# Performance work log

Measured on AMD Instinct MI355X. Metric: run time of the kernel, lower is better.

Reference implementation:

```python
import jax, jax.numpy as jnp
import numpy as np

H = 16
D_MODEL = 1024
D_K = D_MODEL // H


def setup_inputs() -> dict:
    key = jax.random.key(0)
    ks = jax.random.split(key, 12)
    B, S = 4, 2048
    scale = 1.0 / np.sqrt(D_MODEL)
    inp = {
        "query": jax.random.normal(ks[0], (B, S, D_MODEL), dtype=jnp.float32),
        "key": jax.random.normal(ks[1], (B, S, D_MODEL), dtype=jnp.float32),
        "value": jax.random.normal(ks[2], (B, S, D_MODEL), dtype=jnp.float32),
        "Wq": jax.random.normal(ks[3], (D_MODEL, D_MODEL), dtype=jnp.float32) * scale,
        "bq": jnp.zeros((D_MODEL,), dtype=jnp.float32),
        "Wk": jax.random.normal(ks[4], (D_MODEL, D_MODEL), dtype=jnp.float32) * scale,
        "bk": jnp.zeros((D_MODEL,), dtype=jnp.float32),
        "Wv": jax.random.normal(ks[5], (D_MODEL, D_MODEL), dtype=jnp.float32) * scale,
        "bv": jnp.zeros((D_MODEL,), dtype=jnp.float32),
        "Wo": jax.random.normal(ks[6], (D_MODEL, D_MODEL), dtype=jnp.float32) * scale,
        "bo": jnp.zeros((D_MODEL,), dtype=jnp.float32),
    }
    return inp


def reference(query, key, value, Wq, bq, Wk, bk, Wv, bv, Wo, bo):
    B, S, _ = query.shape
    # Linear projections (torch Linear: x @ W^T + b), then split heads -> [B,H,S,d_k]
    def proj(x, W, b):
        y = x @ W.T + b
        return y.reshape(B, S, H, D_K).transpose(0, 2, 1, 3)

    q = proj(query, Wq, bq)
    k = proj(key, Wk, bk)
    v = proj(value, Wv, bv)

    # Explicit QK^T / sqrt(d_k), softmax, AV (no mask; dropout = identity in eval)
    scores = jnp.einsum("bhqd,bhkd->bhqk", q, k) / jnp.sqrt(jnp.float32(D_K))
    attn = jax.nn.softmax(scores, axis=-1)
    x = jnp.einsum("bhqk,bhkd->bhqd", attn, v)

    # Merge heads and final output projection
    x = x.transpose(0, 2, 1, 3).reshape(B, S, H * D_K)
    return x @ Wo.T + bo
```

## Files before the change

### kernel.cpp

```cpp
#include <hip/hip_runtime.h>
#include <hip/hip_bf16.h>
#include <stdint.h>

#define BATCH 4
#define SEQ   2048
#define DM    1024
#define NH    16
#define DK    64
#define MROWS (BATCH * SEQ)

#define C1 0.1803368801111204f

typedef __attribute__((ext_vector_type(8))) short short8;
typedef __attribute__((ext_vector_type(4))) float f32x4;
typedef __attribute__((ext_vector_type(4))) float floatv4;
typedef __attribute__((ext_vector_type(4))) unsigned short us4;
typedef __attribute__((ext_vector_type(4))) unsigned int uint4v;

static __device__ __forceinline__ unsigned short f2bf(float f) {
    union { float f; uint32_t u; } c; c.f = f;
    uint32_t u = c.u;
    return (unsigned short)((u + 0x7fffu + ((u >> 16) & 1u)) >> 16);
}

static __device__ __forceinline__ unsigned int cvt_pk_bf16(float a, float b) {
    __hip_bfloat162 h = __float22bfloat162_rn(float2{a, b});
    unsigned int u; __builtin_memcpy(&u, &h, 4); return u;
}

static __device__ __forceinline__ float ex2(float x) { return __builtin_amdgcn_exp2f(x); }

#define AS1C(p) ((const __attribute__((address_space(1))) unsigned int*)(uintptr_t)(const void*)(p))
#define AS3(p)  ((__attribute__((address_space(3))) unsigned int*)(uintptr_t)(void*)(p))

__global__ __launch_bounds__(256) void cvt3_k(const float* __restrict__ a, const float* __restrict__ b,
                                              const float* __restrict__ c,
                                              unsigned short* __restrict__ oa, unsigned short* __restrict__ ob,
                                              unsigned short* __restrict__ oc) {
    const int z = blockIdx.y;
    const float* s = (z == 0) ? a : (z == 1) ? b : c;
    unsigned short* o = (z == 0) ? oa : (z == 1) ? ob : oc;
    int i = blockIdx.x * 256 + threadIdx.x;
    floatv4 v = ((const floatv4*)s)[i];
    us4 w; w.x = f2bf(v.x); w.y = f2bf(v.y); w.z = f2bf(v.z); w.w = f2bf(v.w);
    ((us4*)o)[i] = w;
}

__global__ __launch_bounds__(256) void cvt4_k(const float* __restrict__ a, const float* __restrict__ b,
                                              const float* __restrict__ c, const float* __restrict__ d,
                                              unsigned short* __restrict__ oa, unsigned short* __restrict__ ob,
                                              unsigned short* __restrict__ oc, unsigned short* __restrict__ od) {
    const int z = blockIdx.y;
    const float* s = (z == 0) ? a : (z == 1) ? b : (z == 2) ? c : d;
    unsigned short* o = (z == 0) ? oa : (z == 1) ? ob : (z == 2) ? oc : od;
    int i = blockIdx.x * 256 + threadIdx.x;
    floatv4 v = ((const floatv4*)s)[i];
    us4 w; w.x = f2bf(v.x); w.y = f2bf(v.y); w.z = f2bf(v.z); w.w = f2bf(v.w);
    ((us4*)o)[i] = w;
}

static __device__ __forceinline__ void gemm_body(const unsigned short* __restrict__ A,
                                                 const unsigned short* __restrict__ Bw,
                                                 const float* __restrict__ bias,
                                                 void* __restrict__ out, int m0, int n0,
                                                 float scale, int mode) {
    constexpr int K = DM;
    constexpr int NK = K / 32;

    const int tid = threadIdx.x;
    const int wave = tid >> 6, lane = tid & 63, quad = lane >> 4, l16 = lane & 15;
    const int wm = wave >> 1, wn = wave & 1;

    __shared__ alignas(16) unsigned short As[2][256 * 32];
    __shared__ alignas(16) unsigned short Bs[2][128 * 32];

    f32x4 acc[4][4];
    #pragma unroll
    for (int i = 0; i < 4; i++)
        #pragma unroll
        for (int j = 0; j < 4; j++) acc[i][j] = (f32x4){0.f, 0.f, 0.f, 0.f};

    const int scol8 = (((lane & 3) ^ ((lane >> 3) & 3))) * 8;
    const unsigned short* Ag0 = A  + (size_t)(m0 + wave * 32 + (lane >> 2)) * K + scol8;
    const unsigned short* Ag1 = Ag0 + (size_t)16 * K;
    const unsigned short* Bg0 = Bw + (size_t)(n0 + wave * 16 + (lane >> 2)) * K + scol8;

    const int rsw = (quad ^ ((l16 >> 1) & 3)) * 8;

    short8 af[4], bfr[4];

#define GX_STG(b, kt)                                                                     \
    {   __builtin_amdgcn_global_load_lds(AS1C(Ag0 + (size_t)(kt) * 32),                   \
                                         AS3(&As[b][(wave * 32) * 32]), 16, 0, 0);        \
        __builtin_amdgcn_global_load_lds(AS1C(Ag1 + (size_t)(kt) * 32),                   \
                                         AS3(&As[b][(wave * 32 + 16) * 32]), 16, 0, 0);   \
        __builtin_amdgcn_global_load_lds(AS1C(Bg0 + (size_t)(kt) * 32),                   \
                                         AS3(&Bs[b][(wave * 16) * 32]), 16, 0, 0); }

#define GX_LD(b)                                                                          \
    {   _Pragma("unroll")                                                                 \
        for (int i_ = 0; i_ < 4; i_++) af[i_]  = *(const short8*)&As[b][(wm * 64 + i_ * 16 + l16) * 32 + rsw]; \
        _Pragma("unroll")                                                                 \
        for (int j_ = 0; j_ < 4; j_++) bfr[j_] = *(const short8*)&Bs[b][(wn * 64 + j_ * 16 + l16) * 32 + rsw]; }

#define GX_MMA                                                                            \
    {   __builtin_amdgcn_s_setprio(1);                                                    \
        _Pragma("unroll")                                                                 \
        for (int i_ = 0; i_ < 4; i_++)                                                    \
            _Pragma("unroll")                                                             \
            for (int j_ = 0; j_ < 4; j_++)                                                \
                acc[i_][j_] = __builtin_amdgcn_mfma_f32_16x16x32_bf16(af[i_], bfr[j_], acc[i_][j_], 0, 0, 0); \
        __builtin_amdgcn_s_setprio(0); }

#define GX_VM0  { asm volatile("s_waitcnt vmcnt(0)" ::: "memory"); }
#define GX_BAR  __builtin_amdgcn_s_barrier()
#define GX_SB0  __builtin_amdgcn_sched_barrier(0)
#define GX_LG0  { asm volatile("s_waitcnt lgkmcnt(0)" ::: "memory"); __builtin_amdgcn_sched_barrier(0); }

    GX_STG(0, 0);
    #pragma unroll 1
    for (int k = 0; k < NK; k += 2) {
        GX_VM0; GX_BAR; GX_SB0;
        GX_STG(1, k + 1);
        GX_LD(0); GX_LG0; GX_MMA;
        GX_VM0; GX_BAR; GX_SB0;
        if (k + 2 < NK) GX_STG(0, k + 2);
        GX_LD(1); GX_LG0; GX_MMA;
    }

#undef GX_STG
#undef GX_LD
#undef GX_MMA
#undef GX_VM0
#undef GX_BAR
#undef GX_SB0
#undef GX_LG0

    #pragma unroll
    for (int nf = 0; nf < 4; nf++) {
        const int n = n0 + wn * 64 + nf * 16 + l16;
        const float bv = bias[n];
        if (mode == 2) {
            const int bb = m0 >> 11;
            const int hh = n >> 6, dd = n & (DK - 1);
            unsigned short* obase = (unsigned short*)out
                                  + (((size_t)bb * NH + hh) * DK + dd) * SEQ
                                  + (m0 & (SEQ - 1)) + wm * 64 + quad * 8;
            #pragma unroll
            for (int mf = 0; mf < 4; mf++) {
                us4 w;
                #pragma unroll
                for (int r = 0; r < 4; r++) w[r] = f2bf(acc[mf][nf][r] + bv);
                *(us4*)(obase + (mf >> 1) * 32 + (mf & 1) * 4) = w;
            }
        } else {
            const int hh = n >> 6, dd = n & (DK - 1);
            #pragma unroll
            for (int mf = 0; mf < 4; mf++) {
                #pragma unroll
                for (int r = 0; r < 4; r++) {
                    const int mrow = m0 + wm * 64 + mf * 16 + quad * 4 + r;
                    float val = (acc[mf][nf][r] + bv) * scale;
                    if (mode == 0) {
                        int bb = mrow >> 11, ss = mrow & (SEQ - 1);
                        ((unsigned short*)out)[((((size_t)bb * NH + hh) * SEQ + ss) << 6) + dd] = f2bf(val);
                    } else {
                        ((float*)out)[(size_t)mrow * DM + n] = val;
                    }
                }
            }
        }
    }
}

__global__ __launch_bounds__(512, 4) void gemm_qkv_k(const unsigned short* qa, const unsigned short* ka,
                                                     const unsigned short* va, const unsigned short* wq,
                                                     const unsigned short* wk, const unsigned short* wv,
                                                     const float* bq, const float* bk, const float* bv,
                                                     unsigned short* qh, unsigned short* kh,
                                                     unsigned short* vtc) {
    const int z = blockIdx.z;
    const unsigned short* A = (z == 0) ? qa : (z == 1) ? ka : va;
    const unsigned short* W = (z == 0) ? wq : (z == 1) ? wk : wv;
    const float* bi = (z == 0) ? bq : (z == 1) ? bk : bv;
    void* o = (z == 0) ? (void*)qh : (z == 1) ? (void*)kh : (void*)vtc;
    const float sc = (z == 0) ? C1 : 1.0f;
    const int mode = (z == 2) ? 2 : 0;
    gemm_body(A, W, bi, o, blockIdx.x * 256, blockIdx.y * 128, sc, mode);
}

__global__ __launch_bounds__(512, 4) void gemm_o_k(const unsigned short* xb, const unsigned short* wo,
                                                   const float* bo, float* out) {
    gemm_body(xb, wo, bo, out, blockIdx.x * 256, blockIdx.y * 128, 1.0f, 1);
}

__global__ __launch_bounds__(256, 2) void flash_attn_k(const unsigned short* __restrict__ Qh,
                                                       const unsigned short* __restrict__ Kh,
                                                       const unsigned short* __restrict__ Vtc,
                                                       unsigned short* __restrict__ Xb) {
    const int tid = threadIdx.x;
    const int wave = tid >> 6, lane = tid & 63, quad = lane >> 4, l16 = lane & 15;
    const int h = blockIdx.y, b = blockIdx.z;
    const unsigned short* Qp = Qh  + (size_t)(b * NH + h) * SEQ * DK;
    const unsigned short* Kp = Kh  + (size_t)(b * NH + h) * SEQ * DK;
    const unsigned short* Vp = Vtc + (size_t)(b * NH + h) * DK * SEQ;
    const int q0 = blockIdx.x * 256 + wave * 64;

    __shared__ alignas(16) unsigned short kt[128][72];
    __shared__ alignas(16) unsigned short vt[64][136];

    short8 aq[4][2];
    #pragma unroll
    for (int m = 0; m < 4; m++)
        #pragma unroll
        for (int kk = 0; kk < 2; kk++)
            aq[m][kk] = *(const short8*)(Qp + (size_t)(q0 + m * 16 + l16) * DK + kk * 32 + quad * 8);

    short8 ones;
    #pragma unroll
    for (int j = 0; j < 8; j++) ones[j] = (short)0x3F80;

    f32x4 O[4][4];
    f32x4 lacc[4];
    #pragma unroll
    for (int m = 0; m < 4; m++) {
        #pragma unroll
        for (int db = 0; db < 4; db++) O[m][db] = (f32x4){0.f, 0.f, 0.f, 0.f};
        lacc[m] = (f32x4){0.f, 0.f, 0.f, 0.f};
    }

    const unsigned short* kgp = Kp + (size_t)(tid >> 3) * DK + (tid & 7) * 8;
    const unsigned short* vgp = Vp + (size_t)(tid >> 4) * SEQ + (tid & 15) * 8;
    unsigned short* kws = &kt[tid >> 3][(tid & 7) * 8];
    unsigned short* vws = &vt[tid >> 4][(tid & 15) * 8];

    short8 krg[4], vrg[4];
    #pragma unroll
    for (int it = 0; it < 4; it++) {
        krg[it] = *(const short8*)(kgp + (size_t)it * 32 * DK);
        vrg[it] = *(const short8*)(vgp + (size_t)it * 16 * SEQ);
    }
    kgp += (size_t)128 * DK;
    vgp += 128;

    for (int t0 = 0; t0 < SEQ; t0 += 128) {
        __syncthreads();
        #pragma unroll
        for (int it = 0; it < 4; it++) {
            *(short8*)(kws + it * 32 * 72) = krg[it];
            *(short8*)(vws + it * 16 * 136) = vrg[it];
        }
        #pragma unroll
        for (int it = 0; it < 4; it++) {
            krg[it] = *(const short8*)(kgp + (size_t)it * 32 * DK);
            vrg[it] = *(const short8*)(vgp + (size_t)it * 16 * SEQ);
        }
        kgp += (size_t)128 * DK;
        vgp += 128;
        asm volatile("s_waitcnt lgkmcnt(0)" ::: "memory");
        __builtin_amdgcn_s_barrier();
        __builtin_amdgcn_sched_barrier(0);

        #pragma unroll
        for (int t = 0; t < 4; t++) {
            f32x4 s[4][2];
            #pragma unroll
            for (int m = 0; m < 4; m++)
                #pragma unroll
                for (int sb = 0; sb < 2; sb++) s[m][sb] = (f32x4){0.f, 0.f, 0.f, 0.f};

            #pragma unroll
            for (int kk = 0; kk < 2; kk++) {
                short8 bk0 = *(const short8*)&kt[(t * 2    ) * 16 + l16][kk * 32 + quad * 8];
                short8 bk1 = *(const short8*)&kt[(t * 2 + 1) * 16 + l16][kk * 32 + quad * 8];
                #pragma unroll
                for (int m = 0; m < 4; m++) {
                    s[m][0] = __builtin_amdgcn_mfma_f32_16x16x32_bf16(bk0, aq[m][kk], s[m][0], 0, 0, 0);
                    s[m][1] = __builtin_amdgcn_mfma_f32_16x16x32_bf16(bk1, aq[m][kk], s[m][1], 0, 0, 0);
                }
            }

            short8 pa[4];
            #pragma unroll
            for (int m = 0; m < 4; m++) {
                uint4v pk;
                pk.x = cvt_pk_bf16(ex2(s[m][0][0]), ex2(s[m][0][1]));
                pk.y = cvt_pk_bf16(ex2(s[m][0][2]), ex2(s[m][0][3]));
                pk.z = cvt_pk_bf16(ex2(s[m][1][0]), ex2(s[m][1][1]));
                pk.w = cvt_pk_bf16(ex2(s[m][1][2]), ex2(s[m][1][3]));
                __builtin_memcpy(&pa[m], &pk, 16);
            }

            #pragma unroll
            for (int db = 0; db < 4; db++) {
                short8 vf = *(const short8*)&vt[db * 16 + l16][t * 32 + quad * 8];
                #pragma unroll
                for (int m = 0; m < 4; m++)
                    O[m][db] = __builtin_amdgcn_mfma_f32_16x16x32_bf16(pa[m], vf, O[m][db], 0, 0, 0);
            }
            #pragma unroll
            for (int m = 0; m < 4; m++)
                lacc[m] = __builtin_amdgcn_mfma_f32_16x16x32_bf16(pa[m], ones, lacc[m], 0, 0, 0);
        }
    }

    #pragma unroll
    for (int m = 0; m < 4; m++) {
        #pragma unroll
        for (int r = 0; r < 4; r++) {
            const float inv = 1.f / lacc[m][r];
            const int srow = q0 + m * 16 + quad * 4 + r;
            unsigned short* op = Xb + ((size_t)b * SEQ + srow) * DM + h * DK;
            #pragma unroll
            for (int db = 0; db < 4; db++)
                op[db * 16 + l16] = f2bf(O[m][db][r] * inv);
        }
    }
}

extern "C" void kernel_launch(void* const* d_in, const int* in_sizes, int n_in,
                              void* d_out, int out_size, void* d_ws, size_t ws_size,
                              hipStream_t stream) {
    const float* q_in = (const float*)d_in[0];
    const float* k_in = (const float*)d_in[1];
    const float* v_in = (const float*)d_in[2];
    const float* Wq   = (const float*)d_in[3];
    const float* bq   = (const float*)d_in[4];
    const float* Wk   = (const float*)d_in[5];
    const float* bk   = (const float*)d_in[6];
    const float* Wv   = (const float*)d_in[7];
    const float* bv   = (const float*)d_in[8];
    const float* Wo   = (const float*)d_in[9];
    const float* bo   = (const float*)d_in[10];

    const size_t MB = 1024ull * 1024ull;
    char* ws = (char*)d_ws;
    unsigned short* qa  = (unsigned short*)(ws +   0 * MB);
    unsigned short* ka  = (unsigned short*)(ws +  16 * MB);
    unsigned short* va  = (unsigned short*)(ws +  32 * MB);
    unsigned short* wqb = (unsigned short*)(ws +  48 * MB);
    unsigned short* wkb = (unsigned short*)(ws +  50 * MB);
    unsigned short* wvb = (unsigned short*)(ws +  52 * MB);
    unsigned short* wob = (unsigned short*)(ws +  54 * MB);
    unsigned short* qh  = (unsigned short*)(ws +  56 * MB);
    unsigned short* kh  = (unsigned short*)(ws +  72 * MB);
    unsigned short* vtc = (unsigned short*)(ws +  88 * MB);
    unsigned short* xb  = (unsigned short*)(ws + 104 * MB);

    cvt3_k<<<dim3(8192, 3), 256, 0, stream>>>(q_in, k_in, v_in, qa, ka, va);
    cvt4_k<<<dim3(1024, 4), 256, 0, stream>>>(Wq, Wk, Wv, Wo, wqb, wkb, wvb, wob);

    gemm_qkv_k<<<dim3(MROWS / 256, DM / 128, 3), 512, 0, stream>>>(qa, ka, va, wqb, wkb, wvb,
                                                                   bq, bk, bv, qh, kh, vtc);

    flash_attn_k<<<dim3(SEQ / 256, NH, BATCH), 256, 0, stream>>>(qh, kh, vtc, xb);

    gemm_o_k<<<dim3(MROWS / 256, DM / 128), 512, 0, stream>>>(xb, wob, bo, (float*)d_out);
}
```

Baseline: 327.0 us.

## Double-buffer K/V tiles in flash attention and merge conversion kernels

The flash attention kernel now keeps two LDS buffers for K and V. The next tile is written into the alternate buffer while the current one is consumed, so each tile needs one barrier instead of two. The two fp32-to-bf16 conversion kernels are also merged into a single launch, which saves one launch overhead. The cost is double the attention LDS use (about 36KB per block), which could limit occupancy, plus an extra prefetch past the end of the sequence on the last tiles.

```diff
diff --git a/kernel.cpp b/kernel.cpp
--- a/kernel.cpp
+++ b/kernel.cpp
@@ -33,29 +33,32 @@
 #define AS1C(p) ((const __attribute__((address_space(1))) unsigned int*)(uintptr_t)(const void*)(p))
 #define AS3(p)  ((__attribute__((address_space(3))) unsigned int*)(uintptr_t)(void*)(p))
 
-__global__ __launch_bounds__(256) void cvt3_k(const float* __restrict__ a, const float* __restrict__ b,
-                                              const float* __restrict__ c,
-                                              unsigned short* __restrict__ oa, unsigned short* __restrict__ ob,
-                                              unsigned short* __restrict__ oc) {
-    const int z = blockIdx.y;
-    const float* s = (z == 0) ? a : (z == 1) ? b : c;
-    unsigned short* o = (z == 0) ? oa : (z == 1) ? ob : oc;
-    int i = blockIdx.x * 256 + threadIdx.x;
-    floatv4 v = ((const floatv4*)s)[i];
-    us4 w; w.x = f2bf(v.x); w.y = f2bf(v.y); w.z = f2bf(v.z); w.w = f2bf(v.w);
-    ((us4*)o)[i] = w;
-}
-
-__global__ __launch_bounds__(256) void cvt4_k(const float* __restrict__ a, const float* __restrict__ b,
-                                              const float* __restrict__ c, const float* __restrict__ d,
-                                              unsigned short* __restrict__ oa, unsigned short* __restrict__ ob,
-                                              unsigned short* __restrict__ oc, unsigned short* __restrict__ od) {
-    const int z = blockIdx.y;
-    const float* s = (z == 0) ? a : (z == 1) ? b : (z == 2) ? c : d;
-    unsigned short* o = (z == 0) ? oa : (z == 1) ? ob : (z == 2) ? oc : od;
-    int i = blockIdx.x * 256 + threadIdx.x;
-    floatv4 v = ((const floatv4*)s)[i];
-    us4 w; w.x = f2bf(v.x); w.y = f2bf(v.y); w.z = f2bf(v.z); w.w = f2bf(v.w);
+__global__ __launch_bounds__(256) void cvt_k(const float* __restrict__ q, const float* __restrict__ k,
+                                             const float* __restrict__ v, const float* __restrict__ wq,
+                                             const float* __restrict__ wk, const float* __restrict__ wv,
+                                             const float* __restrict__ wo,
+                                             unsigned short* __restrict__ oq, unsigned short* __restrict__ ok,
+                                             unsigned short* __restrict__ ov, unsigned short* __restrict__ owq,
+                                             unsigned short* __restrict__ owk, unsigned short* __restrict__ owv,
+                                             unsigned short* __restrict__ owo) {
+    const int bid = blockIdx.x;
+    const float* s;
+    unsigned short* o;
+    int i;
+    if (bid < 24576) {
+        const int z = bid >> 13;
+        i = (bid & 8191) * 256 + threadIdx.x;
+        s = (z == 0) ? q : (z == 1) ? k : v;
+        o = (z == 0) ? oq : (z == 1) ? ok : ov;
+    } else {
+        const int r = bid - 24576;
+        const int z = r >> 10;
+        i = (r & 1023) * 256 + threadIdx.x;
+        s = (z == 0) ? wq : (z == 1) ? wk : (z == 2) ? wv : wo;
+        o = (z == 0) ? owq : (z == 1) ? owk : (z == 2) ? owv : owo;
+    }
+    floatv4 vv = ((const floatv4*)s)[i];
+    us4 w; w.x = f2bf(vv.x); w.y = f2bf(vv.y); w.z = f2bf(vv.z); w.w = f2bf(vv.w);
     ((us4*)o)[i] = w;
 }
 
@@ -206,8 +209,8 @@
     const unsigned short* Vp = Vtc + (size_t)(b * NH + h) * DK * SEQ;
     const int q0 = blockIdx.x * 256 + wave * 64;
 
-    __shared__ alignas(16) unsigned short kt[128][72];
-    __shared__ alignas(16) unsigned short vt[64][136];
+    __shared__ alignas(16) unsigned short kt[2][128][72];
+    __shared__ alignas(16) unsigned short vt[2][64][136];
 
     short8 aq[4][2];
     #pragma unroll
@@ -231,8 +234,8 @@
 
     const unsigned short* kgp = Kp + (size_t)(tid >> 3) * DK + (tid & 7) * 8;
     const unsigned short* vgp = Vp + (size_t)(tid >> 4) * SEQ + (tid & 15) * 8;
-    unsigned short* kws = &kt[tid >> 3][(tid & 7) * 8];
-    unsigned short* vws = &vt[tid >> 4][(tid & 15) * 8];
+    unsigned short* kws0 = &kt[0][tid >> 3][(tid & 7) * 8];
+    unsigned short* vws0 = &vt[0][tid >> 4][(tid & 15) * 8];
 
     short8 krg[4], vrg[4];
     #pragma unroll
@@ -242,67 +245,85 @@
     }
     kgp += (size_t)128 * DK;
     vgp += 128;
-
-    for (int t0 = 0; t0 < SEQ; t0 += 128) {
-        __syncthreads();
-        #pragma unroll
-        for (int it = 0; it < 4; it++) {
-            *(short8*)(kws + it * 32 * 72) = krg[it];
-            *(short8*)(vws + it * 16 * 136) = vrg[it];
-        }
-        #pragma unroll
-        for (int it = 0; it < 4; it++) {
-            krg[it] = *(const short8*)(kgp + (size_t)it * 32 * DK);
-            vrg[it] = *(const short8*)(vgp + (size_t)it * 16 * SEQ);
-        }
-        kgp += (size_t)128 * DK;
-        vgp += 128;
-        asm volatile("s_waitcnt lgkmcnt(0)" ::: "memory");
-        __builtin_amdgcn_s_barrier();
-        __builtin_amdgcn_sched_barrier(0);
-
-        #pragma unroll
-        for (int t = 0; t < 4; t++) {
-            f32x4 s[4][2];
-            #pragma unroll
-            for (int m = 0; m < 4; m++)
-                #pragma unroll
-                for (int sb = 0; sb < 2; sb++) s[m][sb] = (f32x4){0.f, 0.f, 0.f, 0.f};
-
-            #pragma unroll
-            for (int kk = 0; kk < 2; kk++) {
-                short8 bk0 = *(const short8*)&kt[(t * 2    ) * 16 + l16][kk * 32 + quad * 8];
-                short8 bk1 = *(const short8*)&kt[(t * 2 + 1) * 16 + l16][kk * 32 + quad * 8];
-                #pragma unroll
-                for (int m = 0; m < 4; m++) {
-                    s[m][0] = __builtin_amdgcn_mfma_f32_16x16x32_bf16(bk0, aq[m][kk], s[m][0], 0, 0, 0);
-                    s[m][1] = __builtin_amdgcn_mfma_f32_16x16x32_bf16(bk1, aq[m][kk], s[m][1], 0, 0, 0);
-                }
-            }
-
-            short8 pa[4];
-            #pragma unroll
-            for (int m = 0; m < 4; m++) {
-                uint4v pk;
-                pk.x = cvt_pk_bf16(ex2(s[m][0][0]), ex2(s[m][0][1]));
-                pk.y = cvt_pk_bf16(ex2(s[m][0][2]), ex2(s[m][0][3]));
-                pk.z = cvt_pk_bf16(ex2(s[m][1][0]), ex2(s[m][1][1]));
-                pk.w = cvt_pk_bf16(ex2(s[m][1][2]), ex2(s[m][1][3]));
-                __builtin_memcpy(&pa[m], &pk, 16);
-            }
-
-            #pragma unroll
-            for (int db = 0; db < 4; db++) {
-                short8 vf = *(const short8*)&vt[db * 16 + l16][t * 32 + quad * 8];
-                #pragma unroll
-                for (int m = 0; m < 4; m++)
-                    O[m][db] = __builtin_amdgcn_mfma_f32_16x16x32_bf16(pa[m], vf, O[m][db], 0, 0, 0);
-            }
-            #pragma unroll
-            for (int m = 0; m < 4; m++)
-                lacc[m] = __builtin_amdgcn_mfma_f32_16x16x32_bf16(pa[m], ones, lacc[m], 0, 0, 0);
-        }
-    }
+    #pragma unroll
+    for (int it = 0; it < 4; it++) {
+        *(short8*)(kws0 + it * 32 * 72) = krg[it];
+        *(short8*)(vws0 + it * 16 * 136) = vrg[it];
+    }
+    #pragma unroll
+    for (int it = 0; it < 4; it++) {
+        krg[it] = *(const short8*)(kgp + (size_t)it * 32 * DK);
+        vrg[it] = *(const short8*)(vgp + (size_t)it * 16 * SEQ);
+    }
+    kgp += (size_t)128 * DK;
+    vgp += 128;
+    asm volatile("s_waitcnt lgkmcnt(0)" ::: "memory");
+    __builtin_amdgcn_s_barrier();
+    __builtin_amdgcn_sched_barrier(0);
+
+#define FLASH_TILE(cur)                                                                   \
+    {   _Pragma("unroll")                                                                 \
+        for (int it = 0; it < 4; it++) {                                                  \
+            *(short8*)(kws0 + ((cur) ^ 1) * 128 * 72 + it * 32 * 72) = krg[it];           \
+            *(short8*)(vws0 + ((cur) ^ 1) * 64 * 136 + it * 16 * 136) = vrg[it];          \
+        }                                                                                 \
+        _Pragma("unroll")                                                                 \
+        for (int it = 0; it < 4; it++) {                                                  \
+            krg[it] = *(const short8*)(kgp + (size_t)it * 32 * DK);                       \
+            vrg[it] = *(const short8*)(vgp + (size_t)it * 16 * SEQ);                      \
+        }                                                                                 \
+        kgp += (size_t)128 * DK;                                                          \
+        vgp += 128;                                                                       \
+        _Pragma("unroll")                                                                 \
+        for (int t = 0; t < 4; t++) {                                                     \
+            f32x4 s[4][2];                                                                \
+            _Pragma("unroll")                                                             \
+            for (int m = 0; m < 4; m++) {                                                 \
+                s[m][0] = (f32x4){0.f, 0.f, 0.f, 0.f};                                    \
+                s[m][1] = (f32x4){0.f, 0.f, 0.f, 0.f};                                    \
+            }                                                                             \
+            _Pragma("unroll")                                                             \
+            for (int kk = 0; kk < 2; kk++) {                                              \
+                short8 bk0 = *(const short8*)&kt[cur][(t * 2    ) * 16 + l16][kk * 32 + quad * 8]; \
+                short8 bk1 = *(const short8*)&kt[cur][(t * 2 + 1) * 16 + l16][kk * 32 + quad * 8]; \
+                _Pragma("unroll")                                                         \
+                for (int m = 0; m < 4; m++) {                                             \
+                    s[m][0] = __builtin_amdgcn_mfma_f32_16x16x32_bf16(bk0, aq[m][kk], s[m][0], 0, 0, 0); \
+                    s[m][1] = __builtin_amdgcn_mfma_f32_16x16x32_bf16(bk1, aq[m][kk], s[m][1], 0, 0, 0); \
+                }                                                                         \
+            }                                                                             \
+            short8 pa[4];                                                                 \
+            _Pragma("unroll")                                                             \
+            for (int m = 0; m < 4; m++) {                                                 \
+                uint4v pk;                                                                \
+                pk.x = cvt_pk_bf16(ex2(s[m][0][0]), ex2(s[m][0][1]));                     \
+                pk.y = cvt_pk_bf16(ex2(s[m][0][2]), ex2(s[m][0][3]));                     \
+                pk.z = cvt_pk_bf16(ex2(s[m][1][0]), ex2(s[m][1][1]));                     \
+                pk.w = cvt_pk_bf16(ex2(s[m][1][2]), ex2(s[m][1][3]));                     \
+                __builtin_memcpy(&pa[m], &pk, 16);                                        \
+            }                                                                             \
+            _Pragma("unroll")                                                             \
+            for (int db = 0; db < 4; db++) {                                              \
+                short8 vf = *(const short8*)&vt[cur][db * 16 + l16][t * 32 + quad * 8];   \
+                _Pragma("unroll")                                                         \
+                for (int m = 0; m < 4; m++)                                               \
+                    O[m][db] = __builtin_amdgcn_mfma_f32_16x16x32_bf16(pa[m], vf, O[m][db], 0, 0, 0); \
+            }                                                                             \
+            _Pragma("unroll")                                                             \
+            for (int m = 0; m < 4; m++)                                                   \
+                lacc[m] = __builtin_amdgcn_mfma_f32_16x16x32_bf16(pa[m], ones, lacc[m], 0, 0, 0); \
+        }                                                                                 \
+        asm volatile("s_waitcnt lgkmcnt(0)" ::: "memory");                                \
+        __builtin_amdgcn_s_barrier();                                                     \
+        __builtin_amdgcn_sched_barrier(0);                                                \
+    }
+
+    #pragma unroll 1
+    for (int ti = 0; ti < SEQ / 128; ti += 2) {
+        FLASH_TILE(0);
+        FLASH_TILE(1);
+    }
+#undef FLASH_TILE
 
     #pragma unroll
     for (int m = 0; m < 4; m++) {
@@ -347,8 +368,8 @@
     unsigned short* vtc = (unsigned short*)(ws +  88 * MB);
     unsigned short* xb  = (unsigned short*)(ws + 104 * MB);
 
-    cvt3_k<<<dim3(8192, 3), 256, 0, stream>>>(q_in, k_in, v_in, qa, ka, va);
-    cvt4_k<<<dim3(1024, 4), 256, 0, stream>>>(Wq, Wk, Wv, Wo, wqb, wkb, wvb, wob);
+    cvt_k<<<dim3(28672), 256, 0, stream>>>(q_in, k_in, v_in, Wq, Wk, Wv, Wo,
+                                           qa, ka, va, wqb, wkb, wvb, wob);
 
     gemm_qkv_k<<<dim3(MROWS / 256, DM / 128, 3), 512, 0, stream>>>(qa, ka, va, wqb, wkb, wvb,
                                                                    bq, bk, bv, qh, kh, vtc);
```

Result: slower. 334.2 us (+2.2%).

## Load K/V fragments directly from global memory in flash attention, remap blocks per XCD

Applied to the files above, without the earlier changes.

The flash attention kernel no longer stages K and V tiles through shared memory with barriers. Each wave now loads its MFMA fragments straight from global memory and relies on L2 caching for reuse across waves and blocks. Block indices are remapped so the blocks of one (batch, head) pair land on the same XCD, which should improve L2 locality. Launch bounds rise to 4 blocks per CU now that no LDS is used. This trades shared-memory reuse for redundant global and L2 traffic with possibly uncoalesced 16-byte loads, and the remap assumes a fixed grid shape.

```diff
diff --git a/kernel.cpp b/kernel.cpp
--- a/kernel.cpp
+++ b/kernel.cpp
@@ -194,20 +194,23 @@
     gemm_body(xb, wo, bo, out, blockIdx.x * 256, blockIdx.y * 128, 1.0f, 1);
 }
 
-__global__ __launch_bounds__(256, 2) void flash_attn_k(const unsigned short* __restrict__ Qh,
+__global__ __launch_bounds__(256, 4) void flash_attn_k(const unsigned short* __restrict__ Qh,
                                                        const unsigned short* __restrict__ Kh,
                                                        const unsigned short* __restrict__ Vtc,
                                                        unsigned short* __restrict__ Xb) {
     const int tid = threadIdx.x;
     const int wave = tid >> 6, lane = tid & 63, quad = lane >> 4, l16 = lane & 15;
-    const int h = blockIdx.y, b = blockIdx.z;
+
+    const int flat = blockIdx.x + (blockIdx.y << 3) + (blockIdx.z << 7);
+    const int xcd  = flat & 7, slot = flat >> 3;
+    const int xblk = slot & 7;
+    const int hb   = xcd * 8 + (slot >> 3);
+    const int h = hb & (NH - 1), b = hb >> 4;
+
     const unsigned short* Qp = Qh  + (size_t)(b * NH + h) * SEQ * DK;
     const unsigned short* Kp = Kh  + (size_t)(b * NH + h) * SEQ * DK;
     const unsigned short* Vp = Vtc + (size_t)(b * NH + h) * DK * SEQ;
-    const int q0 = blockIdx.x * 256 + wave * 64;
-
-    __shared__ alignas(16) unsigned short kt[128][72];
-    __shared__ alignas(16) unsigned short vt[64][136];
+    const int q0 = xblk * 256 + wave * 64;
 
     short8 aq[4][2];
     #pragma unroll
@@ -229,79 +232,49 @@
         lacc[m] = (f32x4){0.f, 0.f, 0.f, 0.f};
     }
 
-    const unsigned short* kgp = Kp + (size_t)(tid >> 3) * DK + (tid & 7) * 8;
-    const unsigned short* vgp = Vp + (size_t)(tid >> 4) * SEQ + (tid & 15) * 8;
-    unsigned short* kws = &kt[tid >> 3][(tid & 7) * 8];
-    unsigned short* vws = &vt[tid >> 4][(tid & 15) * 8];
-
-    short8 krg[4], vrg[4];
-    #pragma unroll
-    for (int it = 0; it < 4; it++) {
-        krg[it] = *(const short8*)(kgp + (size_t)it * 32 * DK);
-        vrg[it] = *(const short8*)(vgp + (size_t)it * 16 * SEQ);
-    }
-    kgp += (size_t)128 * DK;
-    vgp += 128;
-
-    for (int t0 = 0; t0 < SEQ; t0 += 128) {
-        __syncthreads();
-        #pragma unroll
-        for (int it = 0; it < 4; it++) {
-            *(short8*)(kws + it * 32 * 72) = krg[it];
-            *(short8*)(vws + it * 16 * 136) = vrg[it];
-        }
-        #pragma unroll
-        for (int it = 0; it < 4; it++) {
-            krg[it] = *(const short8*)(kgp + (size_t)it * 32 * DK);
-            vrg[it] = *(const short8*)(vgp + (size_t)it * 16 * SEQ);
-        }
-        kgp += (size_t)128 * DK;
-        vgp += 128;
-        asm volatile("s_waitcnt lgkmcnt(0)" ::: "memory");
-        __builtin_amdgcn_s_barrier();
-        __builtin_amdgcn_sched_barrier(0);
-
-        #pragma unroll
-        for (int t = 0; t < 4; t++) {
-            f32x4 s[4][2];
+    const unsigned short* kfp = Kp + (size_t)l16 * DK + quad * 8;
+    const unsigned short* vfp = Vp + (size_t)l16 * SEQ + quad * 8;
+
+    #pragma unroll 2
+    for (int c = 0; c < SEQ / 32; ++c) {
+        f32x4 s[4][2];
+        #pragma unroll
+        for (int m = 0; m < 4; m++) {
+            s[m][0] = (f32x4){0.f, 0.f, 0.f, 0.f};
+            s[m][1] = (f32x4){0.f, 0.f, 0.f, 0.f};
+        }
+        #pragma unroll
+        for (int kk = 0; kk < 2; kk++) {
+            short8 bk0 = *(const short8*)(kfp + ((size_t)c * 32     ) * DK + kk * 32);
+            short8 bk1 = *(const short8*)(kfp + ((size_t)c * 32 + 16) * DK + kk * 32);
+            #pragma unroll
+            for (int m = 0; m < 4; m++) {
+                s[m][0] = __builtin_amdgcn_mfma_f32_16x16x32_bf16(bk0, aq[m][kk], s[m][0], 0, 0, 0);
+                s[m][1] = __builtin_amdgcn_mfma_f32_16x16x32_bf16(bk1, aq[m][kk], s[m][1], 0, 0, 0);
+            }
+        }
+
+        short8 pa[4];
+        #pragma unroll
+        for (int m = 0; m < 4; m++) {
+            uint4v pk;
+            pk.x = cvt_pk_bf16(ex2(s[m][0][0]), ex2(s[m][0][1]));
+            pk.y = cvt_pk_bf16(ex2(s[m][0][2]), ex2(s[m][0][3]));
+            pk.z = cvt_pk_bf16(ex2(s[m][1][0]), ex2(s[m][1][1]));
+            pk.w = cvt_pk_bf16(ex2(s[m][1][2]), ex2(s[m][1][3]));
+            __builtin_memcpy(&pa[m], &pk, 16);
+        }
+
+        #pragma unroll
+        for (int db = 0; db < 4; db++) {
+            short8 vf = *(const short8*)(vfp + (size_t)db * 16 * SEQ + c * 32);
             #pragma unroll
             for (int m = 0; m < 4; m++)
-                #pragma unroll
-                for (int sb = 0; sb < 2; sb++) s[m][sb] = (f32x4){0.f, 0.f, 0.f, 0.f};
-
-            #pragma unroll
-            for (int kk = 0; kk < 2; kk++) {
-                short8 bk0 = *(const short8*)&kt[(t * 2    ) * 16 + l16][kk * 32 + quad * 8];
-                short8 bk1 = *(const short8*)&kt[(t * 2 + 1) * 16 + l16][kk * 32 + quad * 8];
-                #pragma unroll
-                for (int m = 0; m < 4; m++) {
-                    s[m][0] = __builtin_amdgcn_mfma_f32_16x16x32_bf16(bk0, aq[m][kk], s[m][0], 0, 0, 0);
-                    s[m][1] = __builtin_amdgcn_mfma_f32_16x16x32_bf16(bk1, aq[m][kk], s[m][1], 0, 0, 0);
-                }
-            }
-
-            short8 pa[4];
-            #pragma unroll
-            for (int m = 0; m < 4; m++) {
-                uint4v pk;
-                pk.x = cvt_pk_bf16(ex2(s[m][0][0]), ex2(s[m][0][1]));
-                pk.y = cvt_pk_bf16(ex2(s[m][0][2]), ex2(s[m][0][3]));
-                pk.z = cvt_pk_bf16(ex2(s[m][1][0]), ex2(s[m][1][1]));
-                pk.w = cvt_pk_bf16(ex2(s[m][1][2]), ex2(s[m][1][3]));
-                __builtin_memcpy(&pa[m], &pk, 16);
-            }
-
-            #pragma unroll
-            for (int db = 0; db < 4; db++) {
-                short8 vf = *(const short8*)&vt[db * 16 + l16][t * 32 + quad * 8];
-                #pragma unroll
-                for (int m = 0; m < 4; m++)
-                    O[m][db] = __builtin_amdgcn_mfma_f32_16x16x32_bf16(pa[m], vf, O[m][db], 0, 0, 0);
-            }
-            #pragma unroll
-            for (int m = 0; m < 4; m++)
-                lacc[m] = __builtin_amdgcn_mfma_f32_16x16x32_bf16(pa[m], ones, lacc[m], 0, 0, 0);
-        }
+                O[m][db] = __builtin_amdgcn_mfma_f32_16x16x32_bf16(pa[m], vf, O[m][db], 0, 0, 0);
+        }
+        #pragma unroll
+        for (int m = 0; m < 4; m++)
+            lacc[m] = __builtin_amdgcn_mfma_f32_16x16x32_bf16(pa[m], ones, lacc[m], 0, 0, 0);
     }
 
     #pragma unroll
```

After: 796.8 us. 144% more time.
